# Kernel optimization log

Hardware: AMD Instinct MI355X
Metric: run time of the kernel (lower is better)

## Reference

```python
import jax, jax.numpy as jnp
import numpy as np

V, E, H = 50000, 300, 256  # vocab, word dim, per-direction hidden (nfeat_sent=2H=512)
B, T = 256, 64
NEG = -1e9


def _lstm_scan(x, mask, w_ih, w_hh, b):
    """x: [T,B,E], mask: [T,B,1] float. Masked steps keep (h,c) unchanged.
    Gate order matches torch.nn.LSTM: i, f, g, o."""
    Bsz = x.shape[1]
    Hd = w_hh.shape[1]
    init = (jnp.zeros((Bsz, Hd), x.dtype), jnp.zeros((Bsz, Hd), x.dtype))

    def step(carry, inp):
        h, c = carry
        xt, mt = inp
        z = xt @ w_ih.T + h @ w_hh.T + b  # [B,4H]
        i, f, g, o = jnp.split(z, 4, axis=-1)
        i = jax.nn.sigmoid(i); f = jax.nn.sigmoid(f)
        g = jnp.tanh(g); o = jax.nn.sigmoid(o)
        c_new = f * c + i * g
        h_new = o * jnp.tanh(c_new)
        c = mt * c_new + (1.0 - mt) * c
        h = mt * h_new + (1.0 - mt) * h
        return (h, c), h

    _, hs = jax.lax.scan(step, init, (x, mask))
    return hs  # [T,B,H]


def setup_inputs() -> dict:
    key = jax.random.key(0)
    ks = jax.random.split(key, 9)
    token_ids = jax.random.randint(ks[0], (B, T), 0, V, dtype=jnp.int32)
    lengths = jax.random.randint(ks[1], (B,), 1, T + 1, dtype=jnp.int32)
    emb = jax.random.normal(ks[2], (V, E), jnp.float32) * 0.1
    s = 0.05
    w_ih_f = jax.random.normal(ks[3], (4 * H, E), jnp.float32) * s
    w_hh_f = jax.random.normal(ks[4], (4 * H, H), jnp.float32) * s
    b_f = jax.random.normal(ks[5], (4 * H,), jnp.float32) * s  # b_ih + b_hh fused
    w_ih_b = jax.random.normal(ks[6], (4 * H, E), jnp.float32) * s
    w_hh_b = jax.random.normal(ks[7], (4 * H, H), jnp.float32) * s
    b_b = jax.random.normal(ks[8], (4 * H,), jnp.float32) * s
    return {"token_ids": token_ids, "lengths": lengths, "emb": emb,
            "w_ih_f": w_ih_f, "w_hh_f": w_hh_f, "b_f": b_f,
            "w_ih_b": w_ih_b, "w_hh_b": w_hh_b, "b_b": b_b}


def reference(token_ids, lengths, emb, w_ih_f, w_hh_f, b_f, w_ih_b, w_hh_b, b_b):
    # Batched equivalent of the per-sentence loop: embed -> biLSTM -> max over time.
    x = emb[token_ids]                              # [B,T,E]
    x = jnp.swapaxes(x, 0, 1)                       # [T,B,E] (time-major)
    valid = (jnp.arange(T)[:, None] < lengths[None, :])  # [T,B]
    mask = valid.astype(x.dtype)[:, :, None]        # [T,B,1]

    h_fwd = _lstm_scan(x, mask, w_ih_f, w_hh_f, b_f)  # [T,B,H]
    # Backward direction: reverse time; masked (pad) steps leave state at zero,
    # so each sentence's backward pass starts exactly at its last real token.
    h_bwd = _lstm_scan(x[::-1], mask[::-1], w_ih_b, w_hh_b, b_b)[::-1]

    out = jnp.concatenate([h_fwd, h_bwd], axis=-1)  # [T,B,2H]
    out = jnp.where(valid[:, :, None], out, NEG)
    return jnp.max(out, axis=0)                     # [B, 2H] == [B, nfeat_sent]
```

## Files before the change

kernel.cpp:

```cpp
#include <hip/hip_runtime.h>
#include <hip/hip_bf16.h>
#include <math.h>

#define VV 50000
#define EE 300
#define HD 256
#define BB 256
#define TT 64
#define NEGV -1e9f

#define OFF_H    0
#define OFF_C    262144
#define OFF_CTR  262144
#define OFF_B2   393216
#define OFF_WHHF 395264
#define OFF_WIHB 919552
#define OFF_ZX   1574912
#define WS_FULL_BYTES ((35129344ULL + 64ULL) * 4ULL)

typedef __attribute__((ext_vector_type(8))) short bf16x8;
typedef __attribute__((ext_vector_type(4))) float f32x4;
typedef __attribute__((ext_vector_type(16))) float f32x16;

__device__ __forceinline__ float sigf(float x) {
  return 1.f / (1.f + __expf(-x));
}
__device__ __forceinline__ float tanhfast(float x) {
  return 1.f - 2.f / (__expf(2.f * x) + 1.f);
}
__device__ __forceinline__ unsigned short f2bf(float f) {
  union { float f; unsigned u; } x;
  x.f = f;
  unsigned r = x.u + 0x7fffu + ((x.u >> 16) & 1u);
  return (unsigned short)(r >> 16);
}

__global__ __launch_bounds__(256) void prep_all(
    const float* __restrict__ whf, const float* __restrict__ whb,
    const float* __restrict__ wif, const float* __restrict__ wib,
    const float* __restrict__ bf, const float* __restrict__ bb,
    float* __restrict__ ws) {
  int idx = blockIdx.x * 256 + threadIdx.x;
  if (idx < 131072) ws[OFF_H + idx] = 0.f;
  if (idx < 2048) {
    ((unsigned int*)(ws + OFF_CTR))[idx] = 0u;
    int dir = idx >> 10, jg = idx & 1023, j = jg >> 2, g = jg & 3;
    ws[OFF_B2 + idx] = (dir ? bb : bf)[g * HD + j];
  }
  if (idx < 65536) {
    int lane = idx & 63, kt = (idx >> 6) & 7, ngrp = (idx >> 9) & 63,
        dir = idx >> 15;
    int n = ngrp * 16 + (lane & 15);
    int j = n >> 2, g = n & 3;
    int k0 = kt * 32 + (lane >> 4) * 8;
    const float* W = dir ? whb : whf;
    const float* src = W + (size_t)((g << 8) + j) * HD + k0;
    union { unsigned short u[8]; uint4 q; } hp, lp;
#pragma unroll
    for (int e = 0; e < 8; ++e) {
      float v = src[e];
      unsigned short hh = f2bf(v);
      union { unsigned u; float f; } hf;
      hf.u = (unsigned)hh << 16;
      hp.u[e] = hh;
      lp.u[e] = f2bf(v - hf.f);
    }
    unsigned short* dst =
        (unsigned short*)(ws + OFF_WHHF) + (size_t)idx * 16;
    *(uint4*)dst = hp.q;
    *(uint4*)(dst + 8) = lp.q;
  }
  if (idx < 655360) {
    int n = idx / 320, k = idx - n * 320;
    int dir = n >> 10, jg = n & 1023, j = jg >> 2, g = jg & 3;
    float v = 0.f;
    if (k < EE) {
      const float* W = dir ? wib : wif;
      v = W[(size_t)((g << 8) + j) * EE + k];
    }
    ((unsigned short*)(ws + OFF_WIHB))[idx] = f2bf(v);
  }
}

__global__ __launch_bounds__(256) void init_kernel(float* __restrict__ ws,
                                                   float* __restrict__ out) {
  int idx = blockIdx.x * 256 + threadIdx.x;
  if (idx < 393216) ws[idx] = 0.f;
  if (idx < BB * 2 * HD) out[idx] = NEGV;
}

__global__ __launch_bounds__(256) void zx_mfma(const int* __restrict__ tok,
                                               const float* __restrict__ emb,
                                               float* __restrict__ ws) {
  __shared__ __align__(16) unsigned short a_sm[64 * 64];
  __shared__ __align__(16) unsigned short b_sm[128 * 64];
  const int tid = threadIdx.x;
  const int m0 = blockIdx.x * 64;
  const int n0 = blockIdx.y * 128;
  const unsigned short* wihb = (const unsigned short*)(ws + OFF_WIHB);
  float* zx = ws + OFF_ZX;
  const int lane = tid & 63;
  const int wv = tid >> 6;
  const int wm = wv >> 1, wn = wv & 1;

  f32x16 acc0, acc1;
#pragma unroll
  for (int i = 0; i < 16; ++i) { acc0[i] = 0.f; acc1[i] = 0.f; }

  const int sm_row = tid >> 2;
  const int sq = tid & 3;
  const int tokv = tok[m0 + sm_row];
  const float* er = emb + (size_t)tokv * EE;
  const int bn = tid >> 1;
  const int bq = tid & 1;
  const unsigned short* bsrc = wihb + (size_t)(n0 + bn) * 320 + bq * 32;

  const int fm = wm * 32 + (lane & 31);
  const int koc = lane >> 5;
  const int fnb = wn * 64 + (lane & 31);

  for (int kc = 0; kc < 5; ++kc) {
    const int k0 = kc * 64;
    {
      union { unsigned short u[8]; uint4 v; } pk;
#pragma unroll
      for (int c = 0; c < 2; ++c) {
#pragma unroll
        for (int e = 0; e < 8; ++e) {
          int k = k0 + sq * 16 + c * 8 + e;
          pk.u[e] = (k < EE) ? f2bf(er[k]) : (unsigned short)0;
        }
        int g = sq * 2 + c;
        int gs = g ^ (sm_row & 7);
        *(uint4*)&a_sm[sm_row * 64 + gs * 8] = pk.v;
      }
    }
    {
      const unsigned short* s = bsrc + k0;
#pragma unroll
      for (int c = 0; c < 4; ++c) {
        int g = bq * 4 + c;
        int gs = g ^ (bn & 7);
        *(uint4*)&b_sm[bn * 64 + gs * 8] = *(const uint4*)(s + c * 8);
      }
    }
    __syncthreads();
    bf16x8 afr[4];
#pragma unroll
    for (int ks = 0; ks < 4; ++ks) {
      int gs = (ks * 2 + koc) ^ (fm & 7);
      afr[ks] = *(const bf16x8*)&a_sm[fm * 64 + gs * 8];
    }
#pragma unroll
    for (int nf = 0; nf < 2; ++nf) {
      int n = fnb + nf * 32;
#pragma unroll
      for (int ks = 0; ks < 4; ++ks) {
        int gs = (ks * 2 + koc) ^ (n & 7);
        bf16x8 bfr = *(const bf16x8*)&b_sm[n * 64 + gs * 8];
        if (nf == 0)
          acc0 = __builtin_amdgcn_mfma_f32_32x32x16_bf16(afr[ks], bfr, acc0, 0, 0, 0);
        else
          acc1 = __builtin_amdgcn_mfma_f32_32x32x16_bf16(afr[ks], bfr, acc1, 0, 0, 0);
      }
    }
    __syncthreads();
  }
#pragma unroll
  for (int nf = 0; nf < 2; ++nf) {
#pragma unroll
    for (int r = 0; r < 16; ++r) {
      float v = (nf == 0) ? acc0[r] : acc1[r];
      int row = (r & 3) + 8 * (r >> 2) + 4 * (lane >> 5);
      int m = m0 + wm * 32 + row;
      int n = n0 + wn * 64 + nf * 32 + (lane & 31);
      zx[(size_t)m * 2048 + n] = v;
    }
  }
}

__global__ __launch_bounds__(512) void lstm_persist(
    const int* __restrict__ lens, float* __restrict__ ws,
    float* __restrict__ out) {
  const int bg = blockIdx.x;
  const int slice = blockIdx.y;
  const int dir = blockIdx.z;
  const int tid = threadIdx.x;
  const int lane = tid & 63;
  const int wv = tid >> 6;

  __shared__ __align__(16) unsigned short afrag[8704];
  __shared__ float z_sm[16][132];

  bf16x8 whi[8], wlo[8];
  {
    const unsigned short* wb = (const unsigned short*)(ws + OFF_WHHF);
    const int ngrp = slice * 8 + wv;
    const unsigned short* p =
        wb + (size_t)(((dir * 64 + ngrp) * 8) * 64 + lane) * 16;
#pragma unroll
    for (int kt = 0; kt < 8; ++kt) {
      whi[kt] = *(const bf16x8*)(p + kt * 1024);
      wlo[kt] = *(const bf16x8*)(p + kt * 1024 + 8);
    }
  }

  const int rg = tid >> 5;
  const int k8 = tid & 31;
  const int jl = tid & 31;
  const int brow = bg * 16 + rg;
  const int len = lens[brow];
  const int j = slice * 32 + jl;
  const float4 bias =
      *(const float4*)(ws + OFF_B2 + dir * 1024 + slice * 128 + jl * 4);
  unsigned int* ctr =
      (unsigned int*)(ws + OFF_CTR) + (size_t)(dir * 16 + bg) * 32;
  const float* zx = ws + OFF_ZX;
  float* hb = ws + OFF_H;
  const size_t zxbase = (size_t)brow * TT;
  const int zxoff = dir * 1024 + slice * 128 + jl * 4;

  float c = 0.f, omax = NEGV, h_prev = 0.f;
  float4 zx4 =
      *(const float4*)(zx + (zxbase + (dir ? TT - 1 : 0)) * 2048 + zxoff);

  const int st_chunk = (k8 & 3) * 17 + rg;
  const int st_kt = k8 >> 2;
  const int ld_r = lane & 15, ld_oct = lane >> 4;
  const int ld_chunk = ld_oct * 17 + ld_r;

  for (int s = 0; s < TT; ++s) {
    const int t = dir ? (TT - 1 - s) : s;
    {
      const unsigned long long* s8 = (const unsigned long long*)(
          hb + (size_t)(((s & 1) * 2 + dir) * 256 + brow) * 256 + k8 * 8);
      unsigned long long u0 =
          __hip_atomic_load(s8 + 0, __ATOMIC_RELAXED, __HIP_MEMORY_SCOPE_AGENT);
      unsigned long long u1 =
          __hip_atomic_load(s8 + 1, __ATOMIC_RELAXED, __HIP_MEMORY_SCOPE_AGENT);
      unsigned long long u2 =
          __hip_atomic_load(s8 + 2, __ATOMIC_RELAXED, __HIP_MEMORY_SCOPE_AGENT);
      unsigned long long u3 =
          __hip_atomic_load(s8 + 3, __ATOMIC_RELAXED, __HIP_MEMORY_SCOPE_AGENT);
      float v[8];
      __builtin_memcpy(&v[0], &u0, 8);
      __builtin_memcpy(&v[2], &u1, 8);
      __builtin_memcpy(&v[4], &u2, 8);
      __builtin_memcpy(&v[6], &u3, 8);
      union { unsigned short u[8]; uint4 q; } hp, lp;
#pragma unroll
      for (int e = 0; e < 8; ++e) {
        unsigned short hh = f2bf(v[e]);
        union { unsigned u; float f; } hf;
        hf.u = (unsigned)hh << 16;
        hp.u[e] = hh;
        lp.u[e] = f2bf(v[e] - hf.f);
      }
      int ch = st_kt * 68 + st_chunk;
      *(uint4*)(afrag + ch * 8) = hp.q;
      *(uint4*)(afrag + 4352 + ch * 8) = lp.q;
    }
    __syncthreads();
    f32x4 acc[4];
#pragma unroll
    for (int i = 0; i < 4; ++i) {
      acc[i][0] = 0.f; acc[i][1] = 0.f; acc[i][2] = 0.f; acc[i][3] = 0.f;
    }
#pragma unroll
    for (int kt = 0; kt < 8; ++kt) {
      int ch = kt * 68 + ld_chunk;
      bf16x8 ahi = *(const bf16x8*)(afrag + ch * 8);
      bf16x8 alo = *(const bf16x8*)(afrag + 4352 + ch * 8);
      f32x4 a = acc[kt & 3];
      a = __builtin_amdgcn_mfma_f32_16x16x32_bf16(ahi, whi[kt], a, 0, 0, 0);
      a = __builtin_amdgcn_mfma_f32_16x16x32_bf16(alo, whi[kt], a, 0, 0, 0);
      a = __builtin_amdgcn_mfma_f32_16x16x32_bf16(ahi, wlo[kt], a, 0, 0, 0);
      acc[kt & 3] = a;
    }
    f32x4 zf = (acc[0] + acc[1]) + (acc[2] + acc[3]);
#pragma unroll
    for (int i = 0; i < 4; ++i)
      z_sm[ld_oct * 4 + i][wv * 16 + ld_r] = zf[i];
    __syncthreads();
    const float4 z4 = *(const float4*)&z_sm[rg][jl * 4];
    float h_out = h_prev;
    if (t < len) {
      float ig = sigf(z4.x + zx4.x + bias.x);
      float fg = sigf(z4.y + zx4.y + bias.y);
      float gg = tanhfast(z4.z + zx4.z + bias.z);
      float og = sigf(z4.w + zx4.w + bias.w);
      c = fg * c + ig * gg;
      float hn = og * tanhfast(c);
      h_out = hn;
      omax = fmaxf(omax, hn);
    }
    h_prev = h_out;
    if (s < TT - 1) {
      float* dst =
          hb + (size_t)(((((s + 1) & 1) * 2 + dir) * 256) + brow) * 256 + j;
      __hip_atomic_store(dst, h_out, __ATOMIC_RELAXED,
                         __HIP_MEMORY_SCOPE_AGENT);
      const int tn = dir ? (TT - 2 - s) : (s + 1);
      float4 zxn = *(const float4*)(zx + (zxbase + tn) * 2048 + zxoff);
      asm volatile("s_waitcnt vmcnt(0)" ::: "memory");
      __syncthreads();
      if (tid == 0) {
        __hip_atomic_fetch_add(ctr, 1u, __ATOMIC_RELAXED,
                               __HIP_MEMORY_SCOPE_AGENT);
      }
      if (tid < 64) {
        const unsigned int target = 8u * (unsigned)(s + 1);
        while (__hip_atomic_load(ctr, __ATOMIC_RELAXED,
                                 __HIP_MEMORY_SCOPE_AGENT) < target) {
        }
      }
      __syncthreads();
      asm volatile("" ::: "memory");
      zx4 = zxn;
    }
  }
  out[(size_t)brow * (2 * HD) + dir * HD + j] = omax;
}

__global__ __launch_bounds__(256) void step_fused(
    const int* __restrict__ tok, const int* __restrict__ lens,
    const float* __restrict__ emb,
    const float* __restrict__ wih_f, const float* __restrict__ whh_f,
    const float* __restrict__ bias_f,
    const float* __restrict__ wih_b, const float* __restrict__ whh_b,
    const float* __restrict__ bias_b,
    float* __restrict__ ws, float* __restrict__ out, int s) {
  const int tid = threadIdx.x;
  const int jt = blockIdx.x, bt = blockIdx.y, dir = blockIdx.z;
  const int j0 = jt * 32, b0g = bt * 16;
  const int t = (dir == 0) ? s : (TT - 1 - s);
  const float* Wih = dir ? wih_b : wih_f;
  const float* Whh = dir ? whh_b : whh_f;
  const float* bias = dir ? bias_b : bias_f;
  const float* hcur = ws + OFF_H + (size_t)((s & 1) * 2 + dir) * BB * HD;
  float* hnxt = ws + OFF_H + (size_t)(((s + 1) & 1) * 2 + dir) * BB * HD;
  float* cbuf = ws + OFF_C + (size_t)dir * BB * HD;

  __shared__ float a_sm[16][64];
  __shared__ float w_sm[64][132];
  __shared__ float z_sm[16][132];

  const int cg = tid & 31, bg = tid >> 5;
  float acc[2][4] = {{0.f, 0.f, 0.f, 0.f}, {0.f, 0.f, 0.f, 0.f}};

  for (int phase = 0; phase < 2; ++phase) {
    const float* W = phase ? Whh : Wih;
    const int K = phase ? HD : EE;
    for (int k0 = 0; k0 < K; k0 += 64) {
      const int klen = (K - k0) < 64 ? (K - k0) : 64;
      {
        int bl = tid >> 4, kk4 = tid & 15;
        if (kk4 * 4 < klen) {
          const float* src;
          if (phase == 0) {
            int tk = tok[(b0g + bl) * TT + t];
            src = emb + (size_t)tk * EE + k0 + kk4 * 4;
          } else {
            src = hcur + (size_t)(b0g + bl) * HD + k0 + kk4 * 4;
          }
          *(float4*)&a_sm[bl][kk4 * 4] = *(const float4*)src;
        }
      }
      for (int i = 0; i < 8; ++i) {
        int e = i * 256 + tid;
        int col = e >> 4, kk4 = e & 15;
        if (kk4 * 4 < klen) {
          int gcol = ((col >> 5) * HD) + j0 + (col & 31);
          float4 v = *(const float4*)(W + (size_t)gcol * K + k0 + kk4 * 4);
          w_sm[kk4 * 4 + 0][col] = v.x;
          w_sm[kk4 * 4 + 1][col] = v.y;
          w_sm[kk4 * 4 + 2][col] = v.z;
          w_sm[kk4 * 4 + 3][col] = v.w;
        }
      }
      __syncthreads();
      for (int k = 0; k < klen; ++k) {
        float a0 = a_sm[bg * 2 + 0][k];
        float a1 = a_sm[bg * 2 + 1][k];
        float4 w = *(const float4*)&w_sm[k][cg * 4];
        acc[0][0] += a0 * w.x; acc[0][1] += a0 * w.y;
        acc[0][2] += a0 * w.z; acc[0][3] += a0 * w.w;
        acc[1][0] += a1 * w.x; acc[1][1] += a1 * w.y;
        acc[1][2] += a1 * w.z; acc[1][3] += a1 * w.w;
      }
      __syncthreads();
    }
  }
  *(float4*)&z_sm[bg * 2 + 0][cg * 4] =
      make_float4(acc[0][0], acc[0][1], acc[0][2], acc[0][3]);
  *(float4*)&z_sm[bg * 2 + 1][cg * 4] =
      make_float4(acc[1][0], acc[1][1], acc[1][2], acc[1][3]);
  __syncthreads();
  for (int pi = 0; pi < 2; ++pi) {
    int p = pi * 256 + tid;
    int bl = p >> 5, jl = p & 31;
    int bglob = b0g + bl, jglob = j0 + jl;
    bool valid = t < lens[bglob];
    float h_old = hcur[(size_t)bglob * HD + jglob];
    float h_out = h_old;
    if (valid) {
      float zi = z_sm[bl][0 + jl] + bias[0 * HD + jglob];
      float zf = z_sm[bl][32 + jl] + bias[1 * HD + jglob];
      float zg = z_sm[bl][64 + jl] + bias[2 * HD + jglob];
      float zo = z_sm[bl][96 + jl] + bias[3 * HD + jglob];
      float ig = sigf(zi), fg = sigf(zf), gg = tanhf(zg), og = sigf(zo);
      float c_old = cbuf[(size_t)bglob * HD + jglob];
      float c_new = fg * c_old + ig * gg;
      float h_new = og * tanhf(c_new);
      cbuf[(size_t)bglob * HD + jglob] = c_new;
      h_out = h_new;
      float* op = out + (size_t)bglob * (2 * HD) + dir * HD + jglob;
      *op = fmaxf(*op, h_new);
    }
    hnxt[(size_t)bglob * HD + jglob] = h_out;
  }
}

extern "C" void kernel_launch(void* const* d_in, const int* in_sizes, int n_in,
                              void* d_out, int out_size, void* d_ws,
                              size_t ws_size, hipStream_t stream) {
  const int* tok = (const int*)d_in[0];
  const int* lens = (const int*)d_in[1];
  const float* emb = (const float*)d_in[2];
  const float* wih_f = (const float*)d_in[3];
  const float* whh_f = (const float*)d_in[4];
  const float* b_f = (const float*)d_in[5];
  const float* wih_b = (const float*)d_in[6];
  const float* whh_b = (const float*)d_in[7];
  const float* b_b = (const float*)d_in[8];
  float* out = (float*)d_out;
  float* ws = (float*)d_ws;

  const bool full = ws_size >= WS_FULL_BYTES;
  if (full) {
    hipLaunchKernelGGL(prep_all, dim3(2560), dim3(256), 0, stream, whh_f,
                       whh_b, wih_f, wih_b, b_f, b_b, ws);
    hipLaunchKernelGGL(zx_mfma, dim3(256, 16), dim3(256), 0, stream, tok, emb,
                       ws);
    hipLaunchKernelGGL(lstm_persist, dim3(16, 8, 2), dim3(512), 0, stream,
                       lens, ws, out);
  } else {
    hipLaunchKernelGGL(init_kernel, dim3(1536), dim3(256), 0, stream, ws, out);
    for (int s = 0; s < TT; ++s) {
      hipLaunchKernelGGL(step_fused, dim3(8, 16, 2), dim3(256), 0, stream, tok,
                         lens, emb, wih_f, whh_f, b_f, wih_b, whh_b, b_b, ws,
                         out, s);
    }
  }
}
```

Measured before the change: 255.2 us.

## Fuse input projection into persistent LSTM kernel, dropping precomputed zx buffer

```diff
diff --git a/kernel.cpp b/kernel.cpp
--- a/kernel.cpp
+++ b/kernel.cpp
@@ -14,13 +14,11 @@
 #define OFF_CTR  262144
 #define OFF_B2   393216
 #define OFF_WHHF 395264
-#define OFF_WIHB 919552
-#define OFF_ZX   1574912
-#define WS_FULL_BYTES ((35129344ULL + 64ULL) * 4ULL)
+#define OFF_WIHF 919552
+#define WS_FULL_BYTES (1247232ULL * 4ULL)
 
 typedef __attribute__((ext_vector_type(8))) short bf16x8;
 typedef __attribute__((ext_vector_type(4))) float f32x4;
-typedef __attribute__((ext_vector_type(16))) float f32x16;
 
 __device__ __forceinline__ float sigf(float x) {
   return 1.f / (1.f + __expf(-x));
@@ -65,20 +63,28 @@
       hp.u[e] = hh;
       lp.u[e] = f2bf(v - hf.f);
     }
-    unsigned short* dst =
-        (unsigned short*)(ws + OFF_WHHF) + (size_t)idx * 16;
+    unsigned short* dst = (unsigned short*)(ws + OFF_WHHF) + (size_t)idx * 16;
     *(uint4*)dst = hp.q;
     *(uint4*)(dst + 8) = lp.q;
   }
-  if (idx < 655360) {
-    int n = idx / 320, k = idx - n * 320;
-    int dir = n >> 10, jg = n & 1023, j = jg >> 2, g = jg & 3;
-    float v = 0.f;
-    if (k < EE) {
-      const float* W = dir ? wib : wif;
-      v = W[(size_t)((g << 8) + j) * EE + k];
-    }
-    ((unsigned short*)(ws + OFF_WIHB))[idx] = f2bf(v);
+  if (idx < 81920) {
+    int lane = idx & 63;
+    int f = idx >> 6;
+    int kt = f % 10;
+    int ngrp = (f / 10) & 63;
+    int dir = f / 640;
+    int n = ngrp * 16 + (lane & 15);
+    int j = n >> 2, g = n & 3;
+    int k0 = kt * 32 + (lane >> 4) * 8;
+    const float* W = dir ? wib : wif;
+    union { unsigned short u[8]; uint4 q; } p;
+#pragma unroll
+    for (int e = 0; e < 8; ++e) {
+      int k = k0 + e;
+      p.u[e] = (k < EE) ? f2bf(W[(size_t)((g << 8) + j) * EE + k])
+                        : (unsigned short)0;
+    }
+    *(uint4*)((unsigned short*)(ws + OFF_WIHF) + (size_t)idx * 8) = p.q;
   }
 }
 
@@ -89,98 +95,9 @@
   if (idx < BB * 2 * HD) out[idx] = NEGV;
 }
 
-__global__ __launch_bounds__(256) void zx_mfma(const int* __restrict__ tok,
-                                               const float* __restrict__ emb,
-                                               float* __restrict__ ws) {
-  __shared__ __align__(16) unsigned short a_sm[64 * 64];
-  __shared__ __align__(16) unsigned short b_sm[128 * 64];
-  const int tid = threadIdx.x;
-  const int m0 = blockIdx.x * 64;
-  const int n0 = blockIdx.y * 128;
-  const unsigned short* wihb = (const unsigned short*)(ws + OFF_WIHB);
-  float* zx = ws + OFF_ZX;
-  const int lane = tid & 63;
-  const int wv = tid >> 6;
-  const int wm = wv >> 1, wn = wv & 1;
-
-  f32x16 acc0, acc1;
-#pragma unroll
-  for (int i = 0; i < 16; ++i) { acc0[i] = 0.f; acc1[i] = 0.f; }
-
-  const int sm_row = tid >> 2;
-  const int sq = tid & 3;
-  const int tokv = tok[m0 + sm_row];
-  const float* er = emb + (size_t)tokv * EE;
-  const int bn = tid >> 1;
-  const int bq = tid & 1;
-  const unsigned short* bsrc = wihb + (size_t)(n0 + bn) * 320 + bq * 32;
-
-  const int fm = wm * 32 + (lane & 31);
-  const int koc = lane >> 5;
-  const int fnb = wn * 64 + (lane & 31);
-
-  for (int kc = 0; kc < 5; ++kc) {
-    const int k0 = kc * 64;
-    {
-      union { unsigned short u[8]; uint4 v; } pk;
-#pragma unroll
-      for (int c = 0; c < 2; ++c) {
-#pragma unroll
-        for (int e = 0; e < 8; ++e) {
-          int k = k0 + sq * 16 + c * 8 + e;
-          pk.u[e] = (k < EE) ? f2bf(er[k]) : (unsigned short)0;
-        }
-        int g = sq * 2 + c;
-        int gs = g ^ (sm_row & 7);
-        *(uint4*)&a_sm[sm_row * 64 + gs * 8] = pk.v;
-      }
-    }
-    {
-      const unsigned short* s = bsrc + k0;
-#pragma unroll
-      for (int c = 0; c < 4; ++c) {
-        int g = bq * 4 + c;
-        int gs = g ^ (bn & 7);
-        *(uint4*)&b_sm[bn * 64 + gs * 8] = *(const uint4*)(s + c * 8);
-      }
-    }
-    __syncthreads();
-    bf16x8 afr[4];
-#pragma unroll
-    for (int ks = 0; ks < 4; ++ks) {
-      int gs = (ks * 2 + koc) ^ (fm & 7);
-      afr[ks] = *(const bf16x8*)&a_sm[fm * 64 + gs * 8];
-    }
-#pragma unroll
-    for (int nf = 0; nf < 2; ++nf) {
-      int n = fnb + nf * 32;
-#pragma unroll
-      for (int ks = 0; ks < 4; ++ks) {
-        int gs = (ks * 2 + koc) ^ (n & 7);
-        bf16x8 bfr = *(const bf16x8*)&b_sm[n * 64 + gs * 8];
-        if (nf == 0)
-          acc0 = __builtin_amdgcn_mfma_f32_32x32x16_bf16(afr[ks], bfr, acc0, 0, 0, 0);
-        else
-          acc1 = __builtin_amdgcn_mfma_f32_32x32x16_bf16(afr[ks], bfr, acc1, 0, 0, 0);
-      }
-    }
-    __syncthreads();
-  }
-#pragma unroll
-  for (int nf = 0; nf < 2; ++nf) {
-#pragma unroll
-    for (int r = 0; r < 16; ++r) {
-      float v = (nf == 0) ? acc0[r] : acc1[r];
-      int row = (r & 3) + 8 * (r >> 2) + 4 * (lane >> 5);
-      int m = m0 + wm * 32 + row;
-      int n = n0 + wn * 64 + nf * 32 + (lane & 31);
-      zx[(size_t)m * 2048 + n] = v;
-    }
-  }
-}
-
 __global__ __launch_bounds__(512) void lstm_persist(
-    const int* __restrict__ lens, float* __restrict__ ws,
+    const int* __restrict__ tok, const int* __restrict__ lens,
+    const float* __restrict__ emb, float* __restrict__ ws,
     float* __restrict__ out) {
   const int bg = blockIdx.x;
   const int slice = blockIdx.y;
@@ -189,20 +106,24 @@
   const int lane = tid & 63;
   const int wv = tid >> 6;
 
-  __shared__ __align__(16) unsigned short afrag[8704];
+  __shared__ __align__(16) unsigned short hfr[8192];
+  __shared__ __align__(16) unsigned short ebuf[2][5120];
   __shared__ float z_sm[16][132];
 
-  bf16x8 whi[8], wlo[8];
+  bf16x8 whi[8], wlo[8], wih[10];
   {
-    const unsigned short* wb = (const unsigned short*)(ws + OFF_WHHF);
     const int ngrp = slice * 8 + wv;
-    const unsigned short* p =
-        wb + (size_t)(((dir * 64 + ngrp) * 8) * 64 + lane) * 16;
+    const unsigned short* p = (const unsigned short*)(ws + OFF_WHHF) +
+                              (size_t)(((dir * 64 + ngrp) * 8) * 64 + lane) * 16;
 #pragma unroll
     for (int kt = 0; kt < 8; ++kt) {
       whi[kt] = *(const bf16x8*)(p + kt * 1024);
       wlo[kt] = *(const bf16x8*)(p + kt * 1024 + 8);
     }
+    const unsigned short* q = (const unsigned short*)(ws + OFF_WIHF) +
+                              (size_t)(((dir * 64 + ngrp) * 10) * 64 + lane) * 8;
+#pragma unroll
+    for (int kt = 0; kt < 10; ++kt) wih[kt] = *(const bf16x8*)(q + kt * 512);
   }
 
   const int rg = tid >> 5;
@@ -215,33 +136,66 @@
       *(const float4*)(ws + OFF_B2 + dir * 1024 + slice * 128 + jl * 4);
   unsigned int* ctr =
       (unsigned int*)(ws + OFF_CTR) + (size_t)(dir * 16 + bg) * 32;
-  const float* zx = ws + OFF_ZX;
   float* hb = ws + OFF_H;
-  const size_t zxbase = (size_t)brow * TT;
-  const int zxoff = dir * 1024 + slice * 128 + jl * 4;
+  const int ld_r = lane & 15, ld_oct = lane >> 4;
+  const int trow = brow * TT;
+  const int o2 = 32 + (k8 & 7);
+  const bool has2 = (k8 < 8);
+  const int slot1 = (k8 >> 2) * 64 + rg * 4 + (k8 & 3);
+  const int slot2 = ((o2 >> 2) * 64) + rg * 4 + (o2 & 3);
 
   float c = 0.f, omax = NEGV, h_prev = 0.f;
-  float4 zx4 =
-      *(const float4*)(zx + (zxbase + (dir ? TT - 1 : 0)) * 2048 + zxoff);
-
-  const int st_chunk = (k8 & 3) * 17 + rg;
-  const int st_kt = k8 >> 2;
-  const int ld_r = lane & 15, ld_oct = lane >> 4;
-  const int ld_chunk = ld_oct * 17 + ld_r;
+
+  {
+    const int t0 = dir ? (TT - 1) : 0;
+    const float* er = emb + (size_t)tok[trow + t0] * EE;
+    float4 a0 = *(const float4*)(er + k8 * 8);
+    float4 a1 = *(const float4*)(er + k8 * 8 + 4);
+    union { unsigned short u[8]; uint4 q; } p;
+    p.u[0] = f2bf(a0.x); p.u[1] = f2bf(a0.y); p.u[2] = f2bf(a0.z);
+    p.u[3] = f2bf(a0.w); p.u[4] = f2bf(a1.x); p.u[5] = f2bf(a1.y);
+    p.u[6] = f2bf(a1.z); p.u[7] = f2bf(a1.w);
+    *(uint4*)&ebuf[0][slot1 * 8] = p.q;
+    if (has2) {
+      float4 b0 = make_float4(0.f, 0.f, 0.f, 0.f);
+      float4 b1 = make_float4(0.f, 0.f, 0.f, 0.f);
+      if (o2 <= 37) b0 = *(const float4*)(er + o2 * 8);
+      if (o2 < 37) b1 = *(const float4*)(er + o2 * 8 + 4);
+      union { unsigned short u[8]; uint4 q; } p2;
+      p2.u[0] = f2bf(b0.x); p2.u[1] = f2bf(b0.y); p2.u[2] = f2bf(b0.z);
+      p2.u[3] = f2bf(b0.w); p2.u[4] = f2bf(b1.x); p2.u[5] = f2bf(b1.y);
+      p2.u[6] = f2bf(b1.z); p2.u[7] = f2bf(b1.w);
+      *(uint4*)&ebuf[0][slot2 * 8] = p2.q;
+    }
+  }
 
   for (int s = 0; s < TT; ++s) {
     const int t = dir ? (TT - 1 - s) : s;
+    const bool nstage = (s < TT - 1);
+    const unsigned long long* s8 = (const unsigned long long*)(
+        hb + (size_t)(((s & 1) * 2 + dir) * 256 + brow) * 256 + k8 * 8);
+    unsigned long long u0 =
+        __hip_atomic_load(s8 + 0, __ATOMIC_RELAXED, __HIP_MEMORY_SCOPE_AGENT);
+    unsigned long long u1 =
+        __hip_atomic_load(s8 + 1, __ATOMIC_RELAXED, __HIP_MEMORY_SCOPE_AGENT);
+    unsigned long long u2 =
+        __hip_atomic_load(s8 + 2, __ATOMIC_RELAXED, __HIP_MEMORY_SCOPE_AGENT);
+    unsigned long long u3 =
+        __hip_atomic_load(s8 + 3, __ATOMIC_RELAXED, __HIP_MEMORY_SCOPE_AGENT);
+    float4 pe0, pe1, qe0, qe1;
+    if (nstage) {
+      const int tn = dir ? (TT - 2 - s) : (s + 1);
+      const float* er = emb + (size_t)tok[trow + tn] * EE;
+      pe0 = *(const float4*)(er + k8 * 8);
+      pe1 = *(const float4*)(er + k8 * 8 + 4);
+      qe0 = make_float4(0.f, 0.f, 0.f, 0.f);
+      qe1 = make_float4(0.f, 0.f, 0.f, 0.f);
+      if (has2) {
+        if (o2 <= 37) qe0 = *(const float4*)(er + o2 * 8);
+        if (o2 < 37) qe1 = *(const float4*)(er + o2 * 8 + 4);
+      }
+    }
     {
-      const unsigned long long* s8 = (const unsigned long long*)(
-          hb + (size_t)(((s & 1) * 2 + dir) * 256 + brow) * 256 + k8 * 8);
-      unsigned long long u0 =
-          __hip_atomic_load(s8 + 0, __ATOMIC_RELAXED, __HIP_MEMORY_SCOPE_AGENT);
-      unsigned long long u1 =
-          __hip_atomic_load(s8 + 1, __ATOMIC_RELAXED, __HIP_MEMORY_SCOPE_AGENT);
-      unsigned long long u2 =
-          __hip_atomic_load(s8 + 2, __ATOMIC_RELAXED, __HIP_MEMORY_SCOPE_AGENT);
-      unsigned long long u3 =
-          __hip_atomic_load(s8 + 3, __ATOMIC_RELAXED, __HIP_MEMORY_SCOPE_AGENT);
       float v[8];
       __builtin_memcpy(&v[0], &u0, 8);
       __builtin_memcpy(&v[2], &u1, 8);
@@ -256,9 +210,8 @@
         hp.u[e] = hh;
         lp.u[e] = f2bf(v[e] - hf.f);
       }
-      int ch = st_kt * 68 + st_chunk;
-      *(uint4*)(afrag + ch * 8) = hp.q;
-      *(uint4*)(afrag + 4352 + ch * 8) = lp.q;
+      *(uint4*)&hfr[slot1 * 8] = hp.q;
+      *(uint4*)&hfr[4096 + slot1 * 8] = lp.q;
     }
     __syncthreads();
     f32x4 acc[4];
@@ -266,11 +219,18 @@
     for (int i = 0; i < 4; ++i) {
       acc[i][0] = 0.f; acc[i][1] = 0.f; acc[i][2] = 0.f; acc[i][3] = 0.f;
     }
+    const unsigned short* eb = ebuf[s & 1];
+#pragma unroll
+    for (int kt = 0; kt < 10; ++kt) {
+      bf16x8 ax = *(const bf16x8*)(eb + (kt * 64 + ld_r * 4 + ld_oct) * 8);
+      acc[kt & 3] =
+          __builtin_amdgcn_mfma_f32_16x16x32_bf16(ax, wih[kt], acc[kt & 3], 0, 0, 0);
+    }
 #pragma unroll
     for (int kt = 0; kt < 8; ++kt) {
-      int ch = kt * 68 + ld_chunk;
-      bf16x8 ahi = *(const bf16x8*)(afrag + ch * 8);
-      bf16x8 alo = *(const bf16x8*)(afrag + 4352 + ch * 8);
+      const int sl = (kt * 64 + ld_r * 4 + ld_oct) * 8;
+      bf16x8 ahi = *(const bf16x8*)(hfr + sl);
+      bf16x8 alo = *(const bf16x8*)(hfr + 4096 + sl);
       f32x4 a = acc[kt & 3];
       a = __builtin_amdgcn_mfma_f32_16x16x32_bf16(ahi, whi[kt], a, 0, 0, 0);
       a = __builtin_amdgcn_mfma_f32_16x16x32_bf16(alo, whi[kt], a, 0, 0, 0);
@@ -285,23 +245,36 @@
     const float4 z4 = *(const float4*)&z_sm[rg][jl * 4];
     float h_out = h_prev;
     if (t < len) {
-      float ig = sigf(z4.x + zx4.x + bias.x);
-      float fg = sigf(z4.y + zx4.y + bias.y);
-      float gg = tanhfast(z4.z + zx4.z + bias.z);
-      float og = sigf(z4.w + zx4.w + bias.w);
+      float ig = sigf(z4.x + bias.x);
+      float fg = sigf(z4.y + bias.y);
+      float gg = tanhfast(z4.z + bias.z);
+      float og = sigf(z4.w + bias.w);
       c = fg * c + ig * gg;
       float hn = og * tanhfast(c);
       h_out = hn;
       omax = fmaxf(omax, hn);
     }
     h_prev = h_out;
-    if (s < TT - 1) {
+    if (nstage) {
       float* dst =
           hb + (size_t)(((((s + 1) & 1) * 2 + dir) * 256) + brow) * 256 + j;
       __hip_atomic_store(dst, h_out, __ATOMIC_RELAXED,
                          __HIP_MEMORY_SCOPE_AGENT);
-      const int tn = dir ? (TT - 2 - s) : (s + 1);
-      float4 zxn = *(const float4*)(zx + (zxbase + tn) * 2048 + zxoff);
+      unsigned short* ebn = ebuf[(s + 1) & 1];
+      {
+        union { unsigned short u[8]; uint4 q; } p;
+        p.u[0] = f2bf(pe0.x); p.u[1] = f2bf(pe0.y); p.u[2] = f2bf(pe0.z);
+        p.u[3] = f2bf(pe0.w); p.u[4] = f2bf(pe1.x); p.u[5] = f2bf(pe1.y);
+        p.u[6] = f2bf(pe1.z); p.u[7] = f2bf(pe1.w);
+        *(uint4*)&ebn[slot1 * 8] = p.q;
+        if (has2) {
+          union { unsigned short u[8]; uint4 q; } p2;
+          p2.u[0] = f2bf(qe0.x); p2.u[1] = f2bf(qe0.y); p2.u[2] = f2bf(qe0.z);
+          p2.u[3] = f2bf(qe0.w); p2.u[4] = f2bf(qe1.x); p2.u[5] = f2bf(qe1.y);
+          p2.u[6] = f2bf(qe1.z); p2.u[7] = f2bf(qe1.w);
+          *(uint4*)&ebn[slot2 * 8] = p2.q;
+        }
+      }
       asm volatile("s_waitcnt vmcnt(0)" ::: "memory");
       __syncthreads();
       if (tid == 0) {
@@ -316,7 +289,6 @@
       }
       __syncthreads();
       asm volatile("" ::: "memory");
-      zx4 = zxn;
     }
   }
   out[(size_t)brow * (2 * HD) + dir * HD + j] = omax;
@@ -438,12 +410,10 @@
 
   const bool full = ws_size >= WS_FULL_BYTES;
   if (full) {
-    hipLaunchKernelGGL(prep_all, dim3(2560), dim3(256), 0, stream, whh_f,
+    hipLaunchKernelGGL(prep_all, dim3(512), dim3(256), 0, stream, whh_f,
                        whh_b, wih_f, wih_b, b_f, b_b, ws);
-    hipLaunchKernelGGL(zx_mfma, dim3(256, 16), dim3(256), 0, stream, tok, emb,
-                       ws);
     hipLaunchKernelGGL(lstm_persist, dim3(16, 8, 2), dim3(512), 0, stream,
-                       lens, ws, out);
+                       tok, lens, emb, ws, out);
   } else {
     hipLaunchKernelGGL(init_kernel, dim3(1536), dim3(256), 0, stream, ws, out);
     for (int s = 0; s < TT; ++s) {
```

Result: faster. 220.3 us (-13.7%).
